# Performance work log

Hardware: AMD Instinct MI355X
Metric: run time of the kernel (lower is better)

The kernel has to match this reference:

```python
import math
import jax, jax.numpy as jnp
import numpy as np

B = 8          # number of graphs in the batch
NMAX = 256     # max nodes per graph (padding size)
K = 128        # num_kernels
H = 32         # num_heads
NTYPE = 101    # max_node_type + 1


def setup_inputs() -> dict:
    key = jax.random.key(0)
    ks = jax.random.split(key, 10)
    sizes = np.asarray(NMAX - np.arange(B) * 16, dtype=np.int32)  # 256,240,...,144 -> ragged
    N = int(sizes.sum())  # 1600
    coord = jax.random.normal(ks[0], (N, 3), dtype=jnp.float32) * 3.0
    node_type = jax.random.randint(ks[1], (N,), 0, NTYPE, dtype=jnp.int32)
    gaussian_means = jax.random.uniform(ks[2], (1, K), minval=0.0, maxval=3.0, dtype=jnp.float32)
    gaussian_stds = jax.random.uniform(ks[3], (1, K), minval=0.0, maxval=3.0, dtype=jnp.float32)
    # nn.Embedding(max_node_type+1, 2) tables; original init is const(0)/const(1),
    # we perturb so the computation is non-degenerate.
    mul_w = jax.random.normal(ks[4], (NTYPE, 2), dtype=jnp.float32) * 0.1
    bias_w = 1.0 + jax.random.normal(ks[5], (NTYPE, 2), dtype=jnp.float32) * 0.1
    W1 = jax.random.normal(ks[6], (K, K), dtype=jnp.float32) / math.sqrt(K)
    b1 = jnp.zeros((K,), dtype=jnp.float32)
    W2 = jax.random.normal(ks[7], (K, H), dtype=jnp.float32) / math.sqrt(K)
    b2 = jnp.zeros((H,), dtype=jnp.float32)
    return {
        "coord": coord,
        "gaussian_means": gaussian_means,
        "gaussian_stds": gaussian_stds,
        "mul_w": mul_w,
        "bias_w": bias_w,
        "W1": W1,
        "b1": b1,
        "W2": W2,
        "b2": b2,
        "node_type": node_type,
        "batch_num_nodes": jnp.asarray(sizes),
    }


def reference(coord, gaussian_means, gaussian_stds, mul_w, bias_w, W1, b1, W2, b2,
              node_type, batch_num_nodes):
    N = coord.shape[0]
    offsets = jnp.concatenate([jnp.zeros((1,), dtype=batch_num_nodes.dtype),
                               jnp.cumsum(batch_num_nodes)[:-1]])
    ar = jnp.arange(NMAX)
    idx = offsets[:, None] + ar[None, :]                     # [B, n] flat node index per graph slot
    valid = ar[None, :] < batch_num_nodes[:, None]           # [B, n] node mask
    idx_c = jnp.clip(idx, 0, N - 1)
    pc = coord[idx_c]                                        # [B, n, 3] padded coords
    pt = node_type[idx_c]                                    # [B, n]

    # pairwise Euclidean distance (torch.cdist p=2), sqrt-safe at 0
    diff = pc[:, :, None, :] - pc[:, None, :, :]             # [B, n, n, 3]
    sq = jnp.sum(diff * diff, axis=-1)                       # [B, n, n]
    nz = sq > 0
    dist = jnp.where(nz, jnp.sqrt(jnp.where(nz, sq, 1.0)), 0.0)

    # outer-sum of per-node (src, dst) scaling embeddings
    mul_e = mul_w[pt]                                        # [B, n, 2]
    bias_e = bias_w[pt]
    mul = mul_e[:, :, None, 0] + mul_e[:, None, :, 1]        # [B, n, n]
    bias = bias_e[:, :, None, 0] + bias_e[:, None, :, 1]
    scaled = mul * dist + bias                               # [B, n, n]

    means = gaussian_means.reshape(-1)                       # [K]
    stds = jnp.abs(gaussian_stds.reshape(-1)) + 0.01         # [K]
    z = (scaled[..., None] - means) / stds                   # [B, n, n, K]
    gk = jnp.exp(-0.5 * z * z) / (-math.sqrt(2.0 * math.pi) * stds)

    h = jax.nn.gelu(gk @ W1 + b1, approximate=False)         # exact gelu like torch F.gelu
    out = h @ W2 + b2                                        # [B, n, n, H]

    pair = valid[:, :, None] & valid[:, None, :]             # padded positions -> -inf
    return jnp.where(pair[..., None], out, -jnp.inf)
```

## Files before the change

kernel.cpp:

```cpp
#include <hip/hip_runtime.h>
#include <math.h>

#define NMAXC 256
#define KC 128
#define HC 32
#define BC 8
#define TP 128
#define NEG_SENTINEL (-1.0e30f)
#define LOG2E 1.4426950408889634f

typedef __bf16 bf16x8 __attribute__((ext_vector_type(8)));
typedef float  f32x16 __attribute__((ext_vector_type(16)));
union FragU { uint4 u; bf16x8 v; };

#if __has_builtin(__builtin_amdgcn_exp2f)
#define EXP2F(x) __builtin_amdgcn_exp2f(x)
#else
#define EXP2F(x) exp2f(x)
#endif

__device__ __forceinline__ unsigned pack2(float lo, float hi) {
    return __builtin_amdgcn_perm(__float_as_uint(hi), __float_as_uint(lo), 0x07060302u);
}

__global__ __launch_bounds__(256) void se3d_prep(const float* __restrict__ W1,
                                                 const float* __restrict__ W2,
                                                 const float* __restrict__ gm,
                                                 const float* __restrict__ gs,
                                                 unsigned* __restrict__ wsu) {
    int t = blockIdx.x * 256 + threadIdx.x;
    if (t < 2048) {
        int fb = t >> 6, lane = t & 63;
        int nt = fb >> 3, ks = fb & 7;
        int n  = nt * 32 + (lane & 31);
        int k0 = ks * 16 + 8 * (lane >> 5);
        unsigned u[4];
#pragma unroll
        for (int p = 0; p < 4; ++p)
            u[p] = pack2(W1[(k0 + 2 * p) * KC + n], W1[(k0 + 2 * p + 1) * KC + n]);
        ((uint4*)wsu)[t] = make_uint4(u[0], u[1], u[2], u[3]);
    } else if (t < 2560) {
        int c = t - 2048;
        int ks = c >> 6, lane = c & 63;
        int n  = lane & 31;
        int k0 = ks * 16 + 8 * (lane >> 5);
        unsigned u[4];
#pragma unroll
        for (int p = 0; p < 4; ++p)
            u[p] = pack2(W2[(k0 + 2 * p) * HC + n], W2[(k0 + 2 * p + 1) * HC + n]);
        ((uint4*)wsu)[2048 + c] = make_uint4(u[0], u[1], u[2], u[3]);
    } else if (t < 2688) {
        int k = t - 2560;
        float inv = 1.0f / (fabsf(gs[k]) + 0.01f);
        float m  = gm[k];
        float A2 = -0.5f * inv * inv * LOG2E;
        float* wf = (float*)wsu + 10240;
        wf[k]       = A2;
        wf[128 + k] = -2.0f * A2 * m;
        wf[256 + k] = A2 * m * m;
        wf[384 + k] = -0.3989422804014327f * inv;
    }
}

__global__ __launch_bounds__(256, 4) void se3d_main(
    const float* __restrict__ coord, const float* __restrict__ mulw,
    const float* __restrict__ biasw, const float* __restrict__ b1,
    const float* __restrict__ b2, const int* __restrict__ ntype,
    const int* __restrict__ bnn, const void* __restrict__ ws,
    float* __restrict__ out)
{
    __shared__ __attribute__((aligned(16))) unsigned short hS[4 * 32 * 136];
    __shared__ float scaled[TP];
    __shared__ int   obase[TP];
    __shared__ float cA[KC], cB[KC], cC[KC], cS[KC];

    const int b = blockIdx.y;
    const int n = bnn[b];
    const int q0 = blockIdx.x * TP;
    const int tid = threadIdx.x;

    if (q0 >= n * n) {
        int v = q0 + (tid >> 1) - n * n;
        int wdt = 256 - n;
        int na = n * wdt;
        int i, j;
        if (v < na) { i = v / wdt; j = n + (v - i * wdt); }
        else        { int vp = v - na; i = n + (vp >> 8); j = vp & 255; }
        float4 s4 = make_float4(NEG_SENTINEL, NEG_SENTINEL, NEG_SENTINEL, NEG_SENTINEL);
        float4* o = (float4*)(out + ((size_t)((b * NMAXC + i) * NMAXC + j)) * HC)
                  + (tid & 1) * 4;
#pragma unroll
        for (int t = 0; t < 4; ++t) o[t] = s4;
        return;
    }

    int off = 0;
    for (int t = 0; t < b; ++t) off += bnn[t];

    const float* wf = (const float*)((const char*)ws + 40960);
    if (tid < KC) {
        cA[tid] = wf[tid];
        cB[tid] = wf[128 + tid];
        cC[tid] = wf[256 + tid];
        cS[tid] = wf[384 + tid];
        int q = q0 + tid;
        int i = q / n;
        int j = q - i * n;
        int gi = off + i, gj = off + j;
        float dx = coord[gi * 3 + 0] - coord[gj * 3 + 0];
        float dy = coord[gi * 3 + 1] - coord[gj * 3 + 1];
        float dz = coord[gi * 3 + 2] - coord[gj * 3 + 2];
        float sq = dx * dx + dy * dy + dz * dz;
        float dist = sq > 0.f ? sqrtf(sq) : 0.f;
        int ti = ntype[gi], tj = ntype[gj];
        scaled[tid] = (mulw[ti * 2 + 0] + mulw[tj * 2 + 1]) * dist
                    + (biasw[ti * 2 + 0] + biasw[tj * 2 + 1]);
        obase[tid]  = ((b * NMAXC + i) * NMAXC + j) * HC;
    }
    __syncthreads();

    const int l = tid & 63, w = tid >> 6;
    const int hi = l >> 5, ln31 = l & 31;
    const int m0 = w * 32;
    const float s = scaled[m0 + ln31];

    const bf16x8* wsW1 = (const bf16x8*)ws;
    const bf16x8* wsW2 = (const bf16x8*)((const char*)ws + 32768);
    const float4* A4 = (const float4*)cA;
    const float4* B4 = (const float4*)cB;
    const float4* C4 = (const float4*)cC;
    const float4* S4 = (const float4*)cS;

    f32x16 acc[4];
#pragma unroll
    for (int nt = 0; nt < 4; ++nt) {
        float b1v = b1[nt * 32 + ln31];
#pragma unroll
        for (int r = 0; r < 16; ++r) acc[nt][r] = b1v;
    }

#pragma unroll
    for (int ks = 0; ks < 8; ++ks) {
        int b4 = ks * 4 + 2 * hi;
        float4 a0 = A4[b4], a1 = A4[b4 + 1];
        float4 q0v = B4[b4], q1 = B4[b4 + 1];
        float4 c0 = C4[b4], c1 = C4[b4 + 1];
        float4 s0 = S4[b4], s1 = S4[b4 + 1];
        float g[8];
        g[0] = s0.x * EXP2F(fmaf(fmaf(a0.x, s, q0v.x), s, c0.x));
        g[1] = s0.y * EXP2F(fmaf(fmaf(a0.y, s, q0v.y), s, c0.y));
        g[2] = s0.z * EXP2F(fmaf(fmaf(a0.z, s, q0v.z), s, c0.z));
        g[3] = s0.w * EXP2F(fmaf(fmaf(a0.w, s, q0v.w), s, c0.w));
        g[4] = s1.x * EXP2F(fmaf(fmaf(a1.x, s, q1.x), s, c1.x));
        g[5] = s1.y * EXP2F(fmaf(fmaf(a1.y, s, q1.y), s, c1.y));
        g[6] = s1.z * EXP2F(fmaf(fmaf(a1.z, s, q1.z), s, c1.z));
        g[7] = s1.w * EXP2F(fmaf(fmaf(a1.w, s, q1.w), s, c1.w));
        FragU a;
        a.u.x = pack2(g[0], g[1]);
        a.u.y = pack2(g[2], g[3]);
        a.u.z = pack2(g[4], g[5]);
        a.u.w = pack2(g[6], g[7]);
#pragma unroll
        for (int nt = 0; nt < 4; ++nt) {
            bf16x8 bb = wsW1[(nt * 8 + ks) * 64 + l];
            acc[nt] = __builtin_amdgcn_mfma_f32_32x32x16_bf16(a.v, bb, acc[nt], 0, 0, 0);
        }
    }

    const float KSG = -1.702f * LOG2E;
    unsigned short* hW = hS + w * (32 * 136);
#pragma unroll
    for (int nt = 0; nt < 4; ++nt) {
#pragma unroll
        for (int r = 0; r < 16; ++r) {
            float x = acc[nt][r];
            float e = EXP2F(x * KSG);
            float gl = x * __builtin_amdgcn_rcpf(1.0f + e);
            int rw = (r & 3) + 8 * (r >> 2) + 4 * hi;
            hW[rw * 136 + nt * 32 + ln31] = (unsigned short)(__float_as_uint(gl) >> 16);
        }
    }

    f32x16 c2;
    {
        float b2v = b2[ln31];
#pragma unroll
        for (int r = 0; r < 16; ++r) c2[r] = b2v;
    }
#pragma unroll
    for (int ks = 0; ks < 8; ++ks) {
        bf16x8 av = *(const bf16x8*)(hW + ln31 * 136 + ks * 16 + 8 * hi);
        bf16x8 bv = wsW2[ks * 64 + l];
        c2 = __builtin_amdgcn_mfma_f32_32x32x16_bf16(av, bv, c2, 0, 0, 0);
    }

#pragma unroll
    for (int r = 0; r < 16; ++r) {
        int m = m0 + (r & 3) + 8 * (r >> 2) + 4 * hi;
        out[(size_t)obase[m] + ln31] = c2[r];
    }
}

extern "C" void kernel_launch(void* const* d_in, const int* in_sizes, int n_in,
                              void* d_out, int out_size, void* d_ws, size_t ws_size,
                              hipStream_t stream) {
    const float* coord = (const float*)d_in[0];
    const float* gm    = (const float*)d_in[1];
    const float* gs    = (const float*)d_in[2];
    const float* mulw  = (const float*)d_in[3];
    const float* biasw = (const float*)d_in[4];
    const float* W1    = (const float*)d_in[5];
    const float* b1    = (const float*)d_in[6];
    const float* W2    = (const float*)d_in[7];
    const float* b2    = (const float*)d_in[8];
    const int* ntype   = (const int*)d_in[9];
    const int* bnn     = (const int*)d_in[10];
    float* out = (float*)d_out;

    hipLaunchKernelGGL(se3d_prep, dim3(11), dim3(256), 0, stream,
                       W1, W2, gm, gs, (unsigned*)d_ws);
    hipLaunchKernelGGL(se3d_main, dim3(NMAXC * NMAXC / TP, BC), dim3(256),
                       0, stream,
                       coord, mulw, biasw, b1, b2, ntype, bnn, d_ws, out);
}
```

Baseline: 119.2 us.

## Transpose MFMA operands so GELU output feeds second GEMM from registers

```diff
diff --git a/kernel.cpp b/kernel.cpp
--- a/kernel.cpp
+++ b/kernel.cpp
@@ -21,6 +21,10 @@
 
 __device__ __forceinline__ unsigned pack2(float lo, float hi) {
     return __builtin_amdgcn_perm(__float_as_uint(hi), __float_as_uint(lo), 0x07060302u);
+}
+
+__device__ __forceinline__ int swap23(int k) {
+    return (k & ~12) | ((k & 4) << 1) | ((k & 8) >> 1);
 }
 
 __global__ __launch_bounds__(256) void se3d_prep(const float* __restrict__ W1,
@@ -46,8 +50,11 @@
         int k0 = ks * 16 + 8 * (lane >> 5);
         unsigned u[4];
 #pragma unroll
-        for (int p = 0; p < 4; ++p)
-            u[p] = pack2(W2[(k0 + 2 * p) * HC + n], W2[(k0 + 2 * p + 1) * HC + n]);
+        for (int p = 0; p < 4; ++p) {
+            int ta = swap23(k0 + 2 * p);
+            int tb = swap23(k0 + 2 * p + 1);
+            u[p] = pack2(W2[ta * HC + n], W2[tb * HC + n]);
+        }
         ((uint4*)wsu)[2048 + c] = make_uint4(u[0], u[1], u[2], u[3]);
     } else if (t < 2688) {
         int k = t - 2560;
@@ -69,7 +76,6 @@
     const int* __restrict__ bnn, const void* __restrict__ ws,
     float* __restrict__ out)
 {
-    __shared__ __attribute__((aligned(16))) unsigned short hS[4 * 32 * 136];
     __shared__ float scaled[TP];
     __shared__ int   obase[TP];
     __shared__ float cA[KC], cB[KC], cC[KC], cS[KC];
@@ -134,9 +140,12 @@
     f32x16 acc[4];
 #pragma unroll
     for (int nt = 0; nt < 4; ++nt) {
-        float b1v = b1[nt * 32 + ln31];
-#pragma unroll
-        for (int r = 0; r < 16; ++r) acc[nt][r] = b1v;
+#pragma unroll
+        for (int g = 0; g < 4; ++g) {
+            float4 t4 = *(const float4*)(b1 + nt * 32 + 8 * g + 4 * hi);
+            acc[nt][4 * g + 0] = t4.x; acc[nt][4 * g + 1] = t4.y;
+            acc[nt][4 * g + 2] = t4.z; acc[nt][4 * g + 3] = t4.w;
+        }
     }
 
 #pragma unroll
@@ -163,41 +172,43 @@
 #pragma unroll
         for (int nt = 0; nt < 4; ++nt) {
             bf16x8 bb = wsW1[(nt * 8 + ks) * 64 + l];
-            acc[nt] = __builtin_amdgcn_mfma_f32_32x32x16_bf16(a.v, bb, acc[nt], 0, 0, 0);
-        }
+            acc[nt] = __builtin_amdgcn_mfma_f32_32x32x16_bf16(bb, a.v, acc[nt], 0, 0, 0);
+        }
+    }
+
+    f32x16 c2;
+#pragma unroll
+    for (int g = 0; g < 4; ++g) {
+        float4 t4 = *(const float4*)(b2 + 8 * g + 4 * hi);
+        c2[4 * g + 0] = t4.x; c2[4 * g + 1] = t4.y;
+        c2[4 * g + 2] = t4.z; c2[4 * g + 3] = t4.w;
     }
 
     const float KSG = -1.702f * LOG2E;
-    unsigned short* hW = hS + w * (32 * 136);
 #pragma unroll
     for (int nt = 0; nt < 4; ++nt) {
+        float v[16];
 #pragma unroll
         for (int r = 0; r < 16; ++r) {
             float x = acc[nt][r];
             float e = EXP2F(x * KSG);
-            float gl = x * __builtin_amdgcn_rcpf(1.0f + e);
-            int rw = (r & 3) + 8 * (r >> 2) + 4 * hi;
-            hW[rw * 136 + nt * 32 + ln31] = (unsigned short)(__float_as_uint(gl) >> 16);
-        }
-    }
-
-    f32x16 c2;
-    {
-        float b2v = b2[ln31];
-#pragma unroll
-        for (int r = 0; r < 16; ++r) c2[r] = b2v;
-    }
-#pragma unroll
-    for (int ks = 0; ks < 8; ++ks) {
-        bf16x8 av = *(const bf16x8*)(hW + ln31 * 136 + ks * 16 + 8 * hi);
-        bf16x8 bv = wsW2[ks * 64 + l];
-        c2 = __builtin_amdgcn_mfma_f32_32x32x16_bf16(av, bv, c2, 0, 0, 0);
-    }
-
-#pragma unroll
-    for (int r = 0; r < 16; ++r) {
-        int m = m0 + (r & 3) + 8 * (r >> 2) + 4 * hi;
-        out[(size_t)obase[m] + ln31] = c2[r];
+            v[r] = x * __builtin_amdgcn_rcpf(1.0f + e);
+        }
+        FragU f0, f1;
+        f0.u.x = pack2(v[0],  v[1]);  f0.u.y = pack2(v[2],  v[3]);
+        f0.u.z = pack2(v[4],  v[5]);  f0.u.w = pack2(v[6],  v[7]);
+        f1.u.x = pack2(v[8],  v[9]);  f1.u.y = pack2(v[10], v[11]);
+        f1.u.z = pack2(v[12], v[13]); f1.u.w = pack2(v[14], v[15]);
+        c2 = __builtin_amdgcn_mfma_f32_32x32x16_bf16(wsW2[(2 * nt + 0) * 64 + l], f0.v, c2, 0, 0, 0);
+        c2 = __builtin_amdgcn_mfma_f32_32x32x16_bf16(wsW2[(2 * nt + 1) * 64 + l], f1.v, c2, 0, 0, 0);
+    }
+
+    const int ob = obase[m0 + ln31];
+    float* op = out + (size_t)ob + 4 * hi;
+#pragma unroll
+    for (int g = 0; g < 4; ++g) {
+        *(float4*)(op + 8 * g) =
+            make_float4(c2[4 * g], c2[4 * g + 1], c2[4 * g + 2], c2[4 * g + 3]);
     }
 }
 
```

Measured after the change: 125.7 us. +5.4%, slower.
